# Kernel optimization log

Measured on AMD Instinct MI355X. Metric: run time of the kernel, lower is better.

## Reference

```python
import jax, jax.numpy as jnp
import numpy as np

B, S, IN, OUT = 4, 2048, 4096, 12288


def setup_inputs() -> dict:
    key = jax.random.key(0)
    k1, k2, k3, k4 = jax.random.split(key, 4)
    x = jax.random.normal(k1, (B, S, IN), dtype=jnp.float32).astype(jnp.float16)
    # int8 quantized weight in [-127, 127]
    w_q = jax.random.randint(k2, (OUT, IN), -127, 128, dtype=jnp.int32).astype(jnp.int8)
    # per-output-channel dequant scale (fp32, positive, small)
    w_scale = (jax.random.uniform(k3, (OUT, 1), dtype=jnp.float32) + 0.5) * 0.01
    bias = (jax.random.normal(k4, (OUT,), dtype=jnp.float32) * 0.02).astype(jnp.float16)
    return {"x": x, "w_q": w_q, "w_scale": w_scale, "bias": bias}


def reference(x, w_q, w_scale, bias):
    # dynamic per-token activation quantization: scale = absmax / 127
    x32 = x.astype(jnp.float32)
    x_scale = jnp.maximum(jnp.max(jnp.abs(x32), axis=-1, keepdims=True), 1e-6) / 127.0  # [B,S,1]
    x_q = jnp.clip(jnp.round(x32 / x_scale), -128, 127).astype(jnp.int8)  # [B,S,IN]
    acc = jnp.einsum("bsi,oi->bso", x_q, w_q, preferred_element_type=jnp.int32)  # [B,S,OUT]
    # fused dequant (per-token scale * per-channel scale) + bias
    out = acc.astype(jnp.float32) * x_scale * w_scale[:, 0]
    out = out + bias.astype(jnp.float32)
    return out.astype(x.dtype)
```

## Files before the change

kernel.cpp:

```cpp
#include <hip/hip_runtime.h>
#include <hip/hip_fp16.h>
#include <stdint.h>

#define M_TOK 8192
#define K_IN  4096
#define N_OUT 12288

#define BM 128
#define BN 128
#define BK 64

typedef int v4i_t __attribute__((ext_vector_type(4)));

__device__ __forceinline__ void load_lds16(const void* g, void* l) {
    __builtin_amdgcn_global_load_lds(
        (const __attribute__((address_space(1))) unsigned int*)g,
        (__attribute__((address_space(3))) unsigned int*)l, 16, 0, 0);
}

__global__ __launch_bounds__(256) void pack_w_kernel(
    const int* __restrict__ wsrc, uint32_t* __restrict__ wdst) {
    const size_t i = (size_t)blockIdx.x * 256 + threadIdx.x;
    const int4 v = ((const int4*)wsrc)[i];
    uint32_t p = (uint32_t)(uint8_t)(int8_t)v.x
               | ((uint32_t)(uint8_t)(int8_t)v.y << 8)
               | ((uint32_t)(uint8_t)(int8_t)v.z << 16)
               | ((uint32_t)(uint8_t)(int8_t)v.w << 24);
    wdst[i] = p;
}

__global__ __launch_bounds__(256) void quant_kernel(
    const float* __restrict__ x, int8_t* __restrict__ xq, float* __restrict__ xs) {
    const int token = blockIdx.x;
    const int tid = threadIdx.x;
    const float4* src = (const float4*)(x + (size_t)token * K_IN);

    float v[16];
#pragma unroll
    for (int c = 0; c < 4; ++c) {
        float4 p = src[tid * 4 + c];
        v[c * 4 + 0] = p.x; v[c * 4 + 1] = p.y;
        v[c * 4 + 2] = p.z; v[c * 4 + 3] = p.w;
    }

    float amax = 0.f;
#pragma unroll
    for (int i = 0; i < 16; ++i) amax = fmaxf(amax, fabsf(v[i]));
#pragma unroll
    for (int off = 32; off >= 1; off >>= 1)
        amax = fmaxf(amax, __shfl_xor(amax, off));

    __shared__ float wmax[4];
    const int wave = tid >> 6, lane = tid & 63;
    if (lane == 0) wmax[wave] = amax;
    __syncthreads();
    amax = fmaxf(fmaxf(wmax[0], wmax[1]), fmaxf(wmax[2], wmax[3]));

    const float scale = fmaxf(amax, 1e-6f) / 127.0f;
    if (tid == 0) xs[token] = scale;

    int8_t q[16];
#pragma unroll
    for (int i = 0; i < 16; ++i) {
        float r = rintf(v[i] / scale);
        r = fminf(fmaxf(r, -128.f), 127.f);
        q[i] = (int8_t)(int)r;
    }
    uint4 packed;
    uint32_t* pw = (uint32_t*)&packed;
#pragma unroll
    for (int w = 0; w < 4; ++w) {
        pw[w] = (uint32_t)(uint8_t)q[w * 4 + 0]
              | ((uint32_t)(uint8_t)q[w * 4 + 1] << 8)
              | ((uint32_t)(uint8_t)q[w * 4 + 2] << 16)
              | ((uint32_t)(uint8_t)q[w * 4 + 3] << 24);
    }
    ((uint4*)(xq + (size_t)token * K_IN))[tid] = packed;
}

__global__ __launch_bounds__(256) void gemm_kernel(
    const int8_t* __restrict__ xq, const float* __restrict__ xs,
    const int8_t* __restrict__ wq, const float* __restrict__ wscale,
    const float* __restrict__ bias, float* __restrict__ out) {
    __shared__ int8_t As[BM * BK];
    __shared__ int8_t Bs[BN * BK];

    const int tid = threadIdx.x;
    const int wave = tid >> 6, lane = tid & 63;
    const int m0 = blockIdx.y * BM, n0 = blockIdx.x * BN;
    const int wr = wave >> 1, wc = wave & 1;

    const int8_t* Ag = xq + (size_t)m0 * K_IN;
    const int8_t* Bg = wq + (size_t)n0 * K_IN;

    const int rowS = tid >> 2;
    const int colS = (tid & 3) * 16;
    const size_t gOff0 = (size_t)rowS * K_IN + colS;
    const size_t gOff1 = (size_t)(rowS + 64) * K_IN + colS;
    int8_t* ldsA0 = As + wave * 1024;
    int8_t* ldsA1 = As + 4096 + wave * 1024;
    int8_t* ldsB0 = Bs + wave * 1024;
    int8_t* ldsB1 = Bs + 4096 + wave * 1024;

    const int fr = lane & 15;
    const int fq = lane >> 4;
    const int aoff = (wr * 64 + fr) * BK + fq * 16;
    const int boff = (wc * 64 + fr) * BK + fq * 16;

    v4i_t acc[4][4] = {};

    for (int k0 = 0; k0 < K_IN; k0 += BK) {
        __syncthreads();
        load_lds16(Ag + gOff0 + k0, ldsA0);
        load_lds16(Ag + gOff1 + k0, ldsA1);
        load_lds16(Bg + gOff0 + k0, ldsB0);
        load_lds16(Bg + gOff1 + k0, ldsB1);
        __syncthreads();

        v4i_t af[4], bf[4];
#pragma unroll
        for (int i = 0; i < 4; ++i)
            af[i] = *(const v4i_t*)(As + aoff + i * 16 * BK);
#pragma unroll
        for (int j = 0; j < 4; ++j)
            bf[j] = *(const v4i_t*)(Bs + boff + j * 16 * BK);
#pragma unroll
        for (int i = 0; i < 4; ++i)
#pragma unroll
            for (int j = 0; j < 4; ++j)
                acc[i][j] = __builtin_amdgcn_mfma_i32_16x16x64_i8(af[i], bf[j], acc[i][j], 0, 0, 0);
    }

    const int col = lane & 15;
    const int rq = lane >> 4;
#pragma unroll
    for (int i = 0; i < 4; ++i) {
        const int mb = m0 + wr * 64 + i * 16 + rq * 4;
        float xsv[4];
#pragma unroll
        for (int r = 0; r < 4; ++r) xsv[r] = xs[mb + r];
#pragma unroll
        for (int j = 0; j < 4; ++j) {
            const int n = n0 + wc * 64 + j * 16 + col;
            const float ws = wscale[n];
            const float bv = bias[n];
#pragma unroll
            for (int r = 0; r < 4; ++r) {
                float o = (float)acc[i][j][r] * xsv[r] * ws + bv;
                o = __half2float(__float2half(o));
                out[(size_t)(mb + r) * N_OUT + n] = o;
            }
        }
    }
}

extern "C" void kernel_launch(void* const* d_in, const int* in_sizes, int n_in,
                              void* d_out, int out_size, void* d_ws, size_t ws_size,
                              hipStream_t stream) {
    const float* x      = (const float*)d_in[0];
    const int*   wq32   = (const int*)d_in[1];
    const float* wscale = (const float*)d_in[2];
    const float* bias   = (const float*)d_in[3];
    float* out = (float*)d_out;

    int8_t* xq  = (int8_t*)d_ws;
    float*  xs  = (float*)((char*)d_ws + (size_t)M_TOK * K_IN);
    int8_t* wq8 = (int8_t*)((char*)d_ws + (size_t)M_TOK * K_IN + 65536);

    pack_w_kernel<<<((size_t)N_OUT * K_IN) / 4 / 256, 256, 0, stream>>>(
        wq32, (uint32_t*)wq8);

    quant_kernel<<<M_TOK, 256, 0, stream>>>(x, xq, xs);

    dim3 grid(N_OUT / BN, M_TOK / BM);
    gemm_kernel<<<grid, dim3(256), 0, stream>>>(xq, xs, wq8, wscale, bias, out);
}
```

Measured before the change: 1.132 ms.

## Rewrite int8 GEMM with 256x256 tiles, multi-stage LDS pipeline, fused prep kernel

Merges the weight pack and activation quant kernels into one launch, with coalesced strided accesses in the quant path. The GEMM moves to 256x256 tiles with 8 waves and 128KB of dynamic LDS. It double-buffers K tiles through direct global-to-LDS loads issued ahead of the MFMA phases, with explicit vmcnt/lgkmcnt waits, barriers and setprio. It also adds an XOR swizzle for LDS bank conflicts and block-index swizzling for L2 locality. In exchange it raises register and LDS pressure and adds fragile hand-tuned wait counts.

```diff
diff --git a/kernel.cpp b/kernel.cpp
--- a/kernel.cpp
+++ b/kernel.cpp
@@ -5,10 +5,6 @@
 #define M_TOK 8192
 #define K_IN  4096
 #define N_OUT 12288
-
-#define BM 128
-#define BN 128
-#define BK 64
 
 typedef int v4i_t __attribute__((ext_vector_type(4)));
 
@@ -18,124 +14,190 @@
         (__attribute__((address_space(3))) unsigned int*)l, 16, 0, 0);
 }
 
-__global__ __launch_bounds__(256) void pack_w_kernel(
-    const int* __restrict__ wsrc, uint32_t* __restrict__ wdst) {
-    const size_t i = (size_t)blockIdx.x * 256 + threadIdx.x;
-    const int4 v = ((const int4*)wsrc)[i];
-    uint32_t p = (uint32_t)(uint8_t)(int8_t)v.x
-               | ((uint32_t)(uint8_t)(int8_t)v.y << 8)
-               | ((uint32_t)(uint8_t)(int8_t)v.z << 16)
-               | ((uint32_t)(uint8_t)(int8_t)v.w << 24);
-    wdst[i] = p;
-}
-
-__global__ __launch_bounds__(256) void quant_kernel(
+#define PACK_BLOCKS 49152
+
+__global__ __launch_bounds__(256) void prep_kernel(
+    const int* __restrict__ wsrc, uint32_t* __restrict__ wdst,
     const float* __restrict__ x, int8_t* __restrict__ xq, float* __restrict__ xs) {
-    const int token = blockIdx.x;
     const int tid = threadIdx.x;
+    const int bid = blockIdx.x;
+    if (bid < PACK_BLOCKS) {
+        const size_t i = (size_t)bid * 256 + tid;
+        const int4 v = ((const int4*)wsrc)[i];
+        wdst[i] = (uint32_t)(uint8_t)(int8_t)v.x
+                | ((uint32_t)(uint8_t)(int8_t)v.y << 8)
+                | ((uint32_t)(uint8_t)(int8_t)v.z << 16)
+                | ((uint32_t)(uint8_t)(int8_t)v.w << 24);
+        return;
+    }
+    const int token = bid - PACK_BLOCKS;
     const float4* src = (const float4*)(x + (size_t)token * K_IN);
-
     float v[16];
 #pragma unroll
     for (int c = 0; c < 4; ++c) {
-        float4 p = src[tid * 4 + c];
+        float4 p = src[c * 256 + tid];
         v[c * 4 + 0] = p.x; v[c * 4 + 1] = p.y;
         v[c * 4 + 2] = p.z; v[c * 4 + 3] = p.w;
     }
-
     float amax = 0.f;
 #pragma unroll
     for (int i = 0; i < 16; ++i) amax = fmaxf(amax, fabsf(v[i]));
 #pragma unroll
     for (int off = 32; off >= 1; off >>= 1)
         amax = fmaxf(amax, __shfl_xor(amax, off));
-
     __shared__ float wmax[4];
     const int wave = tid >> 6, lane = tid & 63;
     if (lane == 0) wmax[wave] = amax;
     __syncthreads();
     amax = fmaxf(fmaxf(wmax[0], wmax[1]), fmaxf(wmax[2], wmax[3]));
-
     const float scale = fmaxf(amax, 1e-6f) / 127.0f;
     if (tid == 0) xs[token] = scale;
 
-    int8_t q[16];
-#pragma unroll
-    for (int i = 0; i < 16; ++i) {
-        float r = rintf(v[i] / scale);
-        r = fminf(fmaxf(r, -128.f), 127.f);
-        q[i] = (int8_t)(int)r;
-    }
-    uint4 packed;
-    uint32_t* pw = (uint32_t*)&packed;
-#pragma unroll
-    for (int w = 0; w < 4; ++w) {
-        pw[w] = (uint32_t)(uint8_t)q[w * 4 + 0]
-              | ((uint32_t)(uint8_t)q[w * 4 + 1] << 8)
-              | ((uint32_t)(uint8_t)q[w * 4 + 2] << 16)
-              | ((uint32_t)(uint8_t)q[w * 4 + 3] << 24);
-    }
-    ((uint4*)(xq + (size_t)token * K_IN))[tid] = packed;
-}
-
-__global__ __launch_bounds__(256) void gemm_kernel(
+    uint32_t* dst = (uint32_t*)(xq + (size_t)token * K_IN);
+#pragma unroll
+    for (int c = 0; c < 4; ++c) {
+        uint32_t w = 0;
+#pragma unroll
+        for (int e = 0; e < 4; ++e) {
+            float r = rintf(v[c * 4 + e] / scale);
+            r = fminf(fmaxf(r, -128.f), 127.f);
+            w |= (uint32_t)(uint8_t)(int8_t)(int)r << (8 * e);
+        }
+        dst[c * 256 + tid] = w;
+    }
+}
+
+__global__ __launch_bounds__(512, 2) void gemm_kernel(
     const int8_t* __restrict__ xq, const float* __restrict__ xs,
     const int8_t* __restrict__ wq, const float* __restrict__ wscale,
     const float* __restrict__ bias, float* __restrict__ out) {
-    __shared__ int8_t As[BM * BK];
-    __shared__ int8_t Bs[BN * BK];
-
-    const int tid = threadIdx.x;
-    const int wave = tid >> 6, lane = tid & 63;
-    const int m0 = blockIdx.y * BM, n0 = blockIdx.x * BN;
-    const int wr = wave >> 1, wc = wave & 1;
+    extern __shared__ char smem[];
+
+    const int tid  = threadIdx.x;
+    const int wid  = tid >> 6, lane = tid & 63;
+    const int wr   = wid >> 2, wc = wid & 3;
+
+    const int bid = blockIdx.x;
+    const int swz = (bid & 7) * 192 + (bid >> 3);
+    const int by  = swz / 48, bx = swz - by * 48;
+    const int m0  = by * 256, n0 = bx * 256;
 
     const int8_t* Ag = xq + (size_t)m0 * K_IN;
     const int8_t* Bg = wq + (size_t)n0 * K_IN;
 
-    const int rowS = tid >> 2;
-    const int colS = (tid & 3) * 16;
-    const size_t gOff0 = (size_t)rowS * K_IN + colS;
-    const size_t gOff1 = (size_t)(rowS + 64) * K_IN + colS;
-    int8_t* ldsA0 = As + wave * 1024;
-    int8_t* ldsA1 = As + 4096 + wave * 1024;
-    int8_t* ldsB0 = Bs + wave * 1024;
-    int8_t* ldsB1 = Bs + 4096 + wave * 1024;
-
-    const int fr = lane & 15;
-    const int fq = lane >> 4;
-    const int aoff = (wr * 64 + fr) * BK + fq * 16;
-    const int boff = (wc * 64 + fr) * BK + fq * 16;
-
-    v4i_t acc[4][4] = {};
-
-    for (int k0 = 0; k0 < K_IN; k0 += BK) {
-        __syncthreads();
-        load_lds16(Ag + gOff0 + k0, ldsA0);
-        load_lds16(Ag + gOff1 + k0, ldsA1);
-        load_lds16(Bg + gOff0 + k0, ldsB0);
-        load_lds16(Bg + gOff1 + k0, ldsB1);
-        __syncthreads();
-
+    const int rl = (lane >> 2) & 15;
+    const int rg = (rl & 0xA) | ((rl & 1) << 2) | ((rl >> 2) & 1);
+    const size_t rowByte = (size_t)(wid * 16 + rg) * K_IN;
+    const int gsw16 = ((lane & 3) ^ ((lane >> 3) & 3)) << 4;
+
+    const int fr = lane & 15, fq = lane >> 4;
+    const int sfr = (fr & 0xA) | ((fr & 1) << 2) | ((fr >> 2) & 1);
+    const int frOff = sfr * 64 + (((fq ^ (sfr >> 1)) & 3) << 4);
+
+    auto stage_half = [&](int h) {
+        const int th = h >> 2, r = h & 3;
+        const int isB = r & 1, kk = r >> 1;
+        const int8_t* G = isB ? Bg : Ag;
+        char* lb = smem + (isB << 16) + ((((th & 1) << 1) | kk) << 14) + (wid << 10);
+        const int8_t* g0 = G + rowByte + th * 128 + (kk << 6) + gsw16;
+        load_lds16(g0, lb);
+        load_lds16(g0 + (size_t)128 * K_IN, lb + 8192);
+    };
+
+    v4i_t acc[8][4] = {};
+
+#pragma unroll
+    for (int h = 0; h < 6; ++h) stage_half(h);
+    asm volatile("s_waitcnt vmcnt(8)" ::: "memory");
+    __builtin_amdgcn_s_barrier();
+    __builtin_amdgcn_sched_barrier(0);
+
+    for (int T = 0; T < 32; ++T) {
+        const int b   = T & 1;
+        const int A0o = b << 15, A1o = A0o + 16384;
+        const int B0o = 65536 + A0o, B1o = 65536 + A1o;
+        const int h0  = 4 * T + 6;
+        const int ab  = (wr << 13) + frOff;
+        const int bb  = (wc << 12) + frOff;
         v4i_t af[4], bf[4];
-#pragma unroll
-        for (int i = 0; i < 4; ++i)
-            af[i] = *(const v4i_t*)(As + aoff + i * 16 * BK);
-#pragma unroll
-        for (int j = 0; j < 4; ++j)
-            bf[j] = *(const v4i_t*)(Bs + boff + j * 16 * BK);
+
+#pragma unroll
+        for (int j = 0; j < 4; ++j) bf[j] = *(const v4i_t*)(smem + B0o + bb + (j << 10));
+#pragma unroll
+        for (int i = 0; i < 4; ++i) af[i] = *(const v4i_t*)(smem + A0o + ab + (i << 10));
+        if (h0 < 128) stage_half(h0);
+        __builtin_amdgcn_s_barrier();
+        asm volatile("s_waitcnt lgkmcnt(0)" ::: "memory");
+        __builtin_amdgcn_sched_barrier(0);
+        __builtin_amdgcn_s_setprio(1);
 #pragma unroll
         for (int i = 0; i < 4; ++i)
 #pragma unroll
             for (int j = 0; j < 4; ++j)
                 acc[i][j] = __builtin_amdgcn_mfma_i32_16x16x64_i8(af[i], bf[j], acc[i][j], 0, 0, 0);
-    }
-
-    const int col = lane & 15;
-    const int rq = lane >> 4;
-#pragma unroll
-    for (int i = 0; i < 4; ++i) {
-        const int mb = m0 + wr * 64 + i * 16 + rq * 4;
+        __builtin_amdgcn_s_setprio(0);
+        __builtin_amdgcn_s_barrier();
+        __builtin_amdgcn_sched_barrier(0);
+
+#pragma unroll
+        for (int i = 0; i < 4; ++i) af[i] = *(const v4i_t*)(smem + A0o + ab + ((i + 4) << 10));
+        if (h0 + 1 < 128) stage_half(h0 + 1);
+        __builtin_amdgcn_s_barrier();
+        asm volatile("s_waitcnt lgkmcnt(0)" ::: "memory");
+        __builtin_amdgcn_sched_barrier(0);
+        __builtin_amdgcn_s_setprio(1);
+#pragma unroll
+        for (int i = 0; i < 4; ++i)
+#pragma unroll
+            for (int j = 0; j < 4; ++j)
+                acc[i + 4][j] = __builtin_amdgcn_mfma_i32_16x16x64_i8(af[i], bf[j], acc[i + 4][j], 0, 0, 0);
+        __builtin_amdgcn_s_setprio(0);
+        if (T < 31) asm volatile("s_waitcnt vmcnt(8)" ::: "memory");
+        else        asm volatile("s_waitcnt vmcnt(0)" ::: "memory");
+        __builtin_amdgcn_s_barrier();
+        __builtin_amdgcn_sched_barrier(0);
+
+#pragma unroll
+        for (int j = 0; j < 4; ++j) bf[j] = *(const v4i_t*)(smem + B1o + bb + (j << 10));
+#pragma unroll
+        for (int i = 0; i < 4; ++i) af[i] = *(const v4i_t*)(smem + A1o + ab + (i << 10));
+        if (h0 + 2 < 128) stage_half(h0 + 2);
+        __builtin_amdgcn_s_barrier();
+        asm volatile("s_waitcnt lgkmcnt(0)" ::: "memory");
+        __builtin_amdgcn_sched_barrier(0);
+        __builtin_amdgcn_s_setprio(1);
+#pragma unroll
+        for (int i = 0; i < 4; ++i)
+#pragma unroll
+            for (int j = 0; j < 4; ++j)
+                acc[i][j] = __builtin_amdgcn_mfma_i32_16x16x64_i8(af[i], bf[j], acc[i][j], 0, 0, 0);
+        __builtin_amdgcn_s_setprio(0);
+        __builtin_amdgcn_s_barrier();
+        __builtin_amdgcn_sched_barrier(0);
+
+#pragma unroll
+        for (int i = 0; i < 4; ++i) af[i] = *(const v4i_t*)(smem + A1o + ab + ((i + 4) << 10));
+        if (h0 + 3 < 128) stage_half(h0 + 3);
+        __builtin_amdgcn_s_barrier();
+        asm volatile("s_waitcnt lgkmcnt(0)" ::: "memory");
+        __builtin_amdgcn_sched_barrier(0);
+        __builtin_amdgcn_s_setprio(1);
+#pragma unroll
+        for (int i = 0; i < 4; ++i)
+#pragma unroll
+            for (int j = 0; j < 4; ++j)
+                acc[i + 4][j] = __builtin_amdgcn_mfma_i32_16x16x64_i8(af[i], bf[j], acc[i + 4][j], 0, 0, 0);
+        __builtin_amdgcn_s_setprio(0);
+        if (T < 30)       asm volatile("s_waitcnt vmcnt(8)" ::: "memory");
+        else if (T == 30) asm volatile("s_waitcnt vmcnt(4)" ::: "memory");
+        __builtin_amdgcn_s_barrier();
+        __builtin_amdgcn_sched_barrier(0);
+    }
+
+    const int col = lane & 15, rq = lane >> 4;
+#pragma unroll
+    for (int i = 0; i < 8; ++i) {
+        const int mb = m0 + wr * 128 + i * 16 + rq * 4;
         float xsv[4];
 #pragma unroll
         for (int r = 0; r < 4; ++r) xsv[r] = xs[mb + r];
@@ -167,11 +229,14 @@
     float*  xs  = (float*)((char*)d_ws + (size_t)M_TOK * K_IN);
     int8_t* wq8 = (int8_t*)((char*)d_ws + (size_t)M_TOK * K_IN + 65536);
 
-    pack_w_kernel<<<((size_t)N_OUT * K_IN) / 4 / 256, 256, 0, stream>>>(
-        wq32, (uint32_t*)wq8);
-
-    quant_kernel<<<M_TOK, 256, 0, stream>>>(x, xq, xs);
-
-    dim3 grid(N_OUT / BN, M_TOK / BM);
-    gemm_kernel<<<grid, dim3(256), 0, stream>>>(xq, xs, wq8, wscale, bias, out);
-}
+    static bool attrDone = false;
+    if (!attrDone) {
+        (void)hipFuncSetAttribute((const void*)gemm_kernel,
+                                  hipFuncAttributeMaxDynamicSharedMemorySize, 131072);
+        attrDone = true;
+    }
+
+    prep_kernel<<<PACK_BLOCKS + M_TOK, 256, 0, stream>>>(wq32, (uint32_t*)wq8, x, xq, xs);
+
+    gemm_kernel<<<dim3(1536), dim3(512), 131072, stream>>>(xq, xs, wq8, wscale, bias, out);
+}
```

Result: faster. 956.7 us (-15.5%).
